# Kernel tuning notes

Hardware: AMD Instinct MI355X
Metric: run time of the kernel (lower is better)

The kernel has to match this reference:

```python
import jax, jax.numpy as jnp
import numpy as np

N = 8192      # nodes
E = 262144    # edges (avg degree 32)
IN_DIM = 512
H1 = 256
H2 = 128


def _graph_conv(x, src, dst, W, b, act):
    """DGL GraphConv with norm='both', allow_zero_in_degree=True.
    h = D_in^{-1/2} * A @ (D_out^{-1/2} * x @ W) + b, then activation.
    Degrees clamped to min 1 (DGL behavior)."""
    ones = jnp.ones((src.shape[0],), dtype=x.dtype)
    deg_out = jax.ops.segment_sum(ones, src, num_segments=N)
    deg_in = jax.ops.segment_sum(ones, dst, num_segments=N)
    norm_src = jnp.maximum(deg_out, 1.0) ** -0.5  # [N]
    norm_dst = jnp.maximum(deg_in, 1.0) ** -0.5   # [N]
    # apply weight before aggregation (out_feats < in_feats, as DGL does)
    h = (x * norm_src[:, None]) @ W               # [N, out]
    agg = jax.ops.segment_sum(h[src], dst, num_segments=N)  # gather-scatter SpMM
    return act(agg * norm_dst[:, None] + b)


def setup_inputs() -> dict:
    key = jax.random.key(0)
    ks = jax.random.split(key, 7)
    features = jax.random.normal(ks[0], (N, IN_DIM), dtype=jnp.float32)
    src = jax.random.randint(ks[1], (E,), 0, N)
    dst = jax.random.randint(ks[2], (E,), 0, N)
    W1 = jax.random.normal(ks[3], (IN_DIM, H1), dtype=jnp.float32) * (1.0 / np.sqrt(IN_DIM))
    b1 = jnp.zeros((H1,), dtype=jnp.float32)
    W2 = jax.random.normal(ks[4], (H1, H2), dtype=jnp.float32) * (1.0 / np.sqrt(H1))
    b2 = jnp.zeros((H2,), dtype=jnp.float32)
    return {"features": features, "src": src, "dst": dst,
            "W1": W1, "b1": b1, "W2": W2, "b2": b2}


def reference(features, src, dst, W1, b1, W2, b2):
    x = _graph_conv(features, src, dst, W1, b1, jax.nn.relu)
    emb = _graph_conv(x, src, dst, W2, b2, lambda a: a)
    logits = jax.nn.sigmoid(emb @ emb.T)  # [N, N] dense reconstruction
    return (emb, logits)
```

## Files before the change

### kernel.cpp

```cpp
#include <hip/hip_runtime.h>

#define NN 8192
#define EE 262144
#define IN_DIM 512
#define HD1 256
#define HD2 128

typedef __attribute__((ext_vector_type(8))) short bf16x8;
typedef __attribute__((ext_vector_type(4))) float f32x4;

__device__ inline unsigned short f2bf(float f) {
    unsigned int u = __builtin_bit_cast(unsigned int, f);
    u += 0x7fffu + ((u >> 16) & 1u);
    return (unsigned short)(u >> 16);
}


__global__ void deg_kernel(const int* __restrict__ src, const int* __restrict__ dst,
                           int* __restrict__ deg_out, int* __restrict__ deg_in) {
    int e = blockIdx.x * blockDim.x + threadIdx.x;
    if (e < EE) {
        atomicAdd(&deg_out[src[e]], 1);
        atomicAdd(&deg_in[dst[e]], 1);
    }
}

__global__ void norm_kernel(const int* __restrict__ deg_out, const int* __restrict__ deg_in,
                            float* __restrict__ norm_src, float* __restrict__ norm_dst) {
    int i = blockIdx.x * blockDim.x + threadIdx.x;
    if (i < NN) {
        int dout = deg_out[i]; if (dout < 1) dout = 1;
        int din  = deg_in[i];  if (din  < 1) din  = 1;
        norm_src[i] = rsqrtf((float)dout);
        norm_dst[i] = rsqrtf((float)din);
    }
}

__global__ void scan_kernel(const int* __restrict__ counts, int* __restrict__ row_start) {
    __shared__ int sums[256];
    int t = threadIdx.x;
    int base = t * 32;
    int local[32];
    int s = 0;
    for (int i = 0; i < 32; i++) { local[i] = s; s += counts[base + i]; }
    sums[t] = s;
    __syncthreads();
    for (int off = 1; off < 256; off <<= 1) {
        int v = (t >= off) ? sums[t - off] : 0;
        __syncthreads();
        sums[t] += v;
        __syncthreads();
    }
    int coff = (t == 0) ? 0 : sums[t - 1];
    for (int i = 0; i < 32; i++) row_start[base + i] = coff + local[i];
    if (t == 255) row_start[NN] = sums[255];
}

__global__ void fill_kernel(const int* __restrict__ src, const int* __restrict__ dst,
                            const int* __restrict__ row_start, int* __restrict__ cursor,
                            int* __restrict__ eidx) {
    int e = blockIdx.x * blockDim.x + threadIdx.x;
    if (e < EE) {
        int d = dst[e];
        int pos = atomicAdd(&cursor[d], 1);
        eidx[row_start[d] + pos] = src[e];
    }
}


__global__ void scale_cast_kernel(const float4* __restrict__ x, const float* __restrict__ norm_src,
                                  ushort4* __restrict__ out) {
    int idx = blockIdx.x * blockDim.x + threadIdx.x;
    if (idx < NN * IN_DIM / 4) {
        float ns = norm_src[idx >> 7];
        float4 v = x[idx];
        ushort4 o;
        o.x = f2bf(v.x * ns); o.y = f2bf(v.y * ns);
        o.z = f2bf(v.z * ns); o.w = f2bf(v.w * ns);
        out[idx] = o;
    }
}

__global__ void transpose_cast_kernel(const float* __restrict__ W, unsigned short* __restrict__ Wt,
                                      int K, int Nc) {
    int idx = blockIdx.x * blockDim.x + threadIdx.x;
    if (idx < K * Nc) {
        int n = idx / K;
        int k = idx - n * K;
        Wt[idx] = f2bf(W[k * Nc + n]);
    }
}

template <int EPI>
__global__ __launch_bounds__(256) void gemm_tn(const short* __restrict__ A,
                                               const short* __restrict__ B,
                                               float* __restrict__ C, int N, int K) {
    int wave = threadIdx.x >> 6;
    int lane = threadIdx.x & 63;
    int wr = wave >> 1, wc = wave & 1;
    int row0 = blockIdx.y * 128 + wr * 64;
    int col0 = blockIdx.x * 128 + wc * 64;
    int l15 = lane & 15, q = lane >> 4;

    f32x4 acc[4][4] = {};
    const short* Abase = A + (size_t)(row0 + l15) * K + q * 8;
    const short* Bbase = B + (size_t)(col0 + l15) * K + q * 8;
    int nk = K >> 5;
    for (int ks = 0; ks < nk; ks++) {
        bf16x8 a[4], b[4];
#pragma unroll
        for (int t = 0; t < 4; t++) {
            a[t] = *(const bf16x8*)(Abase + (size_t)t * 16 * K + ks * 32);
            b[t] = *(const bf16x8*)(Bbase + (size_t)t * 16 * K + ks * 32);
        }
#pragma unroll
        for (int ti = 0; ti < 4; ti++)
#pragma unroll
            for (int tj = 0; tj < 4; tj++)
                acc[ti][tj] = __builtin_amdgcn_mfma_f32_16x16x32_bf16(a[ti], b[tj], acc[ti][tj], 0, 0, 0);
    }
#pragma unroll
    for (int ti = 0; ti < 4; ti++) {
#pragma unroll
        for (int tj = 0; tj < 4; tj++) {
#pragma unroll
            for (int r = 0; r < 4; r++) {
                int row = row0 + ti * 16 + q * 4 + r;
                int col = col0 + tj * 16 + l15;
                float v = acc[ti][tj][r];
                if (EPI == 1) v = __builtin_amdgcn_rcpf(1.0f + __expf(-v));
                C[(size_t)row * N + col] = v;
            }
        }
    }
}


__global__ void spmm1_kernel(const float* __restrict__ h1, const int* __restrict__ row_start,
                             const int* __restrict__ eidx, const float* __restrict__ norm_dst,
                             const float* __restrict__ norm_src, const float* __restrict__ b1,
                             unsigned short* __restrict__ x1n) {
    int r = blockIdx.x;
    int t = threadIdx.x;
    int s = row_start[r], e = row_start[r + 1];
    float sum = 0.0f;
    int i = s;
    for (; i + 4 <= e; i += 4) {
        int n0 = eidx[i], n1 = eidx[i + 1], n2 = eidx[i + 2], n3 = eidx[i + 3];
        float v0 = h1[n0 * HD1 + t];
        float v1 = h1[n1 * HD1 + t];
        float v2 = h1[n2 * HD1 + t];
        float v3 = h1[n3 * HD1 + t];
        sum += v0 + v1 + v2 + v3;
    }
    for (; i < e; i++) sum += h1[eidx[i] * HD1 + t];
    float x = sum * norm_dst[r] + b1[t];
    x = fmaxf(x, 0.0f) * norm_src[r];
    x1n[r * HD1 + t] = f2bf(x);
}

__global__ void spmm2_kernel(const float* __restrict__ h2, const int* __restrict__ row_start,
                             const int* __restrict__ eidx, const float* __restrict__ norm_dst,
                             const float* __restrict__ b2, float* __restrict__ emb,
                             unsigned short* __restrict__ embb) {
    int r = blockIdx.x;
    int t = threadIdx.x;
    int s = row_start[r], e = row_start[r + 1];
    float sum = 0.0f;
    int i = s;
    for (; i + 4 <= e; i += 4) {
        int n0 = eidx[i], n1 = eidx[i + 1], n2 = eidx[i + 2], n3 = eidx[i + 3];
        float v0 = h2[n0 * HD2 + t];
        float v1 = h2[n1 * HD2 + t];
        float v2 = h2[n2 * HD2 + t];
        float v3 = h2[n3 * HD2 + t];
        sum += v0 + v1 + v2 + v3;
    }
    for (; i < e; i++) sum += h2[eidx[i] * HD2 + t];
    float x = sum * norm_dst[r] + b2[t];
    emb[r * HD2 + t] = x;
    embb[r * HD2 + t] = f2bf(x);
}


extern "C" void kernel_launch(void* const* d_in, const int* in_sizes, int n_in,
                              void* d_out, int out_size, void* d_ws, size_t ws_size,
                              hipStream_t stream) {
    const float* features = (const float*)d_in[0];
    const int* src = (const int*)d_in[1];
    const int* dst = (const int*)d_in[2];
    const float* W1 = (const float*)d_in[3];
    const float* b1 = (const float*)d_in[4];
    const float* W2 = (const float*)d_in[5];
    const float* b2 = (const float*)d_in[6];

    char* ws = (char*)d_ws;
    size_t o = 0;
    auto alloc = [&](size_t bytes) -> char* {
        char* p = ws + o;
        o = (o + bytes + 255) & ~(size_t)255;
        return p;
    };
    int* deg_out = (int*)alloc(NN * 4);
    int* deg_in  = (int*)alloc(NN * 4);
    int* cursor  = (int*)alloc(NN * 4);
    float* norm_src = (float*)alloc(NN * 4);
    float* norm_dst = (float*)alloc(NN * 4);
    int* row_start  = (int*)alloc((NN + 1) * 4);
    int* eidx       = (int*)alloc(EE * 4);
    unsigned short* xn  = (unsigned short*)alloc((size_t)NN * IN_DIM * 2);
    unsigned short* w1t = (unsigned short*)alloc((size_t)HD1 * IN_DIM * 2);
    unsigned short* w2t = (unsigned short*)alloc((size_t)HD2 * HD1 * 2);
    float* h1 = (float*)alloc((size_t)NN * HD1 * 4);
    unsigned short* x1n = (unsigned short*)alloc((size_t)NN * HD1 * 2);
    float* h2 = (float*)alloc((size_t)NN * HD2 * 4);
    unsigned short* embb = (unsigned short*)alloc((size_t)NN * HD2 * 2);

    float* emb_out = (float*)d_out;
    float* logits_out = emb_out + (size_t)NN * HD2;

    hipMemsetAsync(deg_out, 0, (size_t)NN * 4 * 3, stream);

    deg_kernel<<<EE / 256, 256, 0, stream>>>(src, dst, deg_out, deg_in);
    norm_kernel<<<NN / 256, 256, 0, stream>>>(deg_out, deg_in, norm_src, norm_dst);
    scan_kernel<<<1, 256, 0, stream>>>(deg_in, row_start);
    fill_kernel<<<EE / 256, 256, 0, stream>>>(src, dst, row_start, cursor, eidx);

    scale_cast_kernel<<<(NN * IN_DIM / 4) / 256, 256, 0, stream>>>(
        (const float4*)features, norm_src, (ushort4*)xn);
    transpose_cast_kernel<<<(IN_DIM * HD1 + 255) / 256, 256, 0, stream>>>(W1, w1t, IN_DIM, HD1);
    transpose_cast_kernel<<<(HD1 * HD2 + 255) / 256, 256, 0, stream>>>(W2, w2t, HD1, HD2);

    gemm_tn<0><<<dim3(HD1 / 128, NN / 128), 256, 0, stream>>>(
        (const short*)xn, (const short*)w1t, h1, HD1, IN_DIM);
    spmm1_kernel<<<NN, HD1, 0, stream>>>(h1, row_start, eidx, norm_dst, norm_src, b1, x1n);

    gemm_tn<0><<<dim3(HD2 / 128, NN / 128), 256, 0, stream>>>(
        (const short*)x1n, (const short*)w2t, h2, HD2, HD1);
    spmm2_kernel<<<NN, HD2, 0, stream>>>(h2, row_start, eidx, norm_dst, b2, emb_out, embb);

    gemm_tn<1><<<dim3(NN / 128, NN / 128), 256, 0, stream>>>(
        (const short*)embb, (const short*)embb, logits_out, NN, HD2);
}
```

Measured before the change: 434.8 us.

## Stage GEMM epilogue through LDS for coalesced stores; vectorize SpMM with wave-per-row

The GEMM epilogue now writes accumulators to shared memory in two halves and then emits coalesced 16-byte row stores, using nontemporal stores for the large sigmoid logits output. The SpMM kernels switch from one block per row with scalar gathers to one wave per row, with float4/float2 vector gathers and vector stores. The aim is to cut write transactions on the 256MB logits output and raise gather efficiency. The cost is extra LDS traffic and barriers in the epilogue.

```diff
diff --git a/kernel.cpp b/kernel.cpp
--- a/kernel.cpp
+++ b/kernel.cpp
@@ -95,6 +95,7 @@
 __global__ __launch_bounds__(256) void gemm_tn(const short* __restrict__ A,
                                                const short* __restrict__ B,
                                                float* __restrict__ C, int N, int K) {
+    __shared__ float lds[64][132];
     int wave = threadIdx.x >> 6;
     int lane = threadIdx.x & 63;
     int wr = wave >> 1, wc = wave & 1;
@@ -119,67 +120,112 @@
             for (int tj = 0; tj < 4; tj++)
                 acc[ti][tj] = __builtin_amdgcn_mfma_f32_16x16x32_bf16(a[ti], b[tj], acc[ti][tj], 0, 0, 0);
     }
-#pragma unroll
-    for (int ti = 0; ti < 4; ti++) {
-#pragma unroll
-        for (int tj = 0; tj < 4; tj++) {
-#pragma unroll
-            for (int r = 0; r < 4; r++) {
-                int row = row0 + ti * 16 + q * 4 + r;
-                int col = col0 + tj * 16 + l15;
-                float v = acc[ti][tj][r];
-                if (EPI == 1) v = __builtin_amdgcn_rcpf(1.0f + __expf(-v));
-                C[(size_t)row * N + col] = v;
+
+    int brow = blockIdx.y * 128;
+    int bcol = blockIdx.x * 128;
+#pragma unroll
+    for (int h = 0; h < 2; h++) {
+        __syncthreads();
+        if (wr == h) {
+#pragma unroll
+            for (int ti = 0; ti < 4; ti++)
+#pragma unroll
+                for (int tj = 0; tj < 4; tj++)
+#pragma unroll
+                    for (int r = 0; r < 4; r++)
+                        lds[ti * 16 + q * 4 + r][wc * 64 + tj * 16 + l15] = acc[ti][tj][r];
+        }
+        __syncthreads();
+#pragma unroll
+        for (int it = 0; it < 8; it++) {
+            int idx = it * 256 + threadIdx.x;
+            int rl = idx >> 5;
+            int c4 = (idx & 31) << 2;
+            f32x4 v = *(const f32x4*)&lds[rl][c4];
+            float* dst = C + (size_t)(brow + h * 64 + rl) * N + bcol + c4;
+            if (EPI == 1) {
+                f32x4 s;
+                s[0] = __builtin_amdgcn_rcpf(1.0f + __expf(-v[0]));
+                s[1] = __builtin_amdgcn_rcpf(1.0f + __expf(-v[1]));
+                s[2] = __builtin_amdgcn_rcpf(1.0f + __expf(-v[2]));
+                s[3] = __builtin_amdgcn_rcpf(1.0f + __expf(-v[3]));
+                __builtin_nontemporal_store(s, (f32x4*)dst);
+            } else {
+                *(f32x4*)dst = v;
             }
         }
     }
 }
 
 
-__global__ void spmm1_kernel(const float* __restrict__ h1, const int* __restrict__ row_start,
-                             const int* __restrict__ eidx, const float* __restrict__ norm_dst,
-                             const float* __restrict__ norm_src, const float* __restrict__ b1,
-                             unsigned short* __restrict__ x1n) {
-    int r = blockIdx.x;
-    int t = threadIdx.x;
+__global__ __launch_bounds__(256) void spmm1_kernel(
+        const float* __restrict__ h1, const int* __restrict__ row_start,
+        const int* __restrict__ eidx, const float* __restrict__ norm_dst,
+        const float* __restrict__ norm_src, const float* __restrict__ b1,
+        unsigned short* __restrict__ x1n) {
+    int wave = threadIdx.x >> 6, lane = threadIdx.x & 63;
+    int r = blockIdx.x * 4 + wave;
     int s = row_start[r], e = row_start[r + 1];
-    float sum = 0.0f;
+    const float* hb = h1 + (size_t)lane * 4;
+    float sx = 0.f, sy = 0.f, sz = 0.f, sw = 0.f;
     int i = s;
     for (; i + 4 <= e; i += 4) {
         int n0 = eidx[i], n1 = eidx[i + 1], n2 = eidx[i + 2], n3 = eidx[i + 3];
-        float v0 = h1[n0 * HD1 + t];
-        float v1 = h1[n1 * HD1 + t];
-        float v2 = h1[n2 * HD1 + t];
-        float v3 = h1[n3 * HD1 + t];
-        sum += v0 + v1 + v2 + v3;
-    }
-    for (; i < e; i++) sum += h1[eidx[i] * HD1 + t];
-    float x = sum * norm_dst[r] + b1[t];
-    x = fmaxf(x, 0.0f) * norm_src[r];
-    x1n[r * HD1 + t] = f2bf(x);
-}
-
-__global__ void spmm2_kernel(const float* __restrict__ h2, const int* __restrict__ row_start,
-                             const int* __restrict__ eidx, const float* __restrict__ norm_dst,
-                             const float* __restrict__ b2, float* __restrict__ emb,
-                             unsigned short* __restrict__ embb) {
-    int r = blockIdx.x;
-    int t = threadIdx.x;
+        float4 v0 = *(const float4*)(hb + (size_t)n0 * HD1);
+        float4 v1 = *(const float4*)(hb + (size_t)n1 * HD1);
+        float4 v2 = *(const float4*)(hb + (size_t)n2 * HD1);
+        float4 v3 = *(const float4*)(hb + (size_t)n3 * HD1);
+        sx += (v0.x + v1.x) + (v2.x + v3.x);
+        sy += (v0.y + v1.y) + (v2.y + v3.y);
+        sz += (v0.z + v1.z) + (v2.z + v3.z);
+        sw += (v0.w + v1.w) + (v2.w + v3.w);
+    }
+    for (; i < e; i++) {
+        float4 v = *(const float4*)(hb + (size_t)eidx[i] * HD1);
+        sx += v.x; sy += v.y; sz += v.z; sw += v.w;
+    }
+    float nd = norm_dst[r], ns = norm_src[r];
+    float4 bb = *(const float4*)(b1 + lane * 4);
+    ushort4 o;
+    o.x = f2bf(fmaxf(sx * nd + bb.x, 0.f) * ns);
+    o.y = f2bf(fmaxf(sy * nd + bb.y, 0.f) * ns);
+    o.z = f2bf(fmaxf(sz * nd + bb.z, 0.f) * ns);
+    o.w = f2bf(fmaxf(sw * nd + bb.w, 0.f) * ns);
+    *(ushort4*)(x1n + (size_t)r * HD1 + lane * 4) = o;
+}
+
+__global__ __launch_bounds__(256) void spmm2_kernel(
+        const float* __restrict__ h2, const int* __restrict__ row_start,
+        const int* __restrict__ eidx, const float* __restrict__ norm_dst,
+        const float* __restrict__ b2, float* __restrict__ emb,
+        unsigned short* __restrict__ embb) {
+    int wave = threadIdx.x >> 6, lane = threadIdx.x & 63;
+    int r = blockIdx.x * 4 + wave;
     int s = row_start[r], e = row_start[r + 1];
-    float sum = 0.0f;
+    const float* hb = h2 + (size_t)lane * 2;
+    float sx = 0.f, sy = 0.f;
     int i = s;
     for (; i + 4 <= e; i += 4) {
         int n0 = eidx[i], n1 = eidx[i + 1], n2 = eidx[i + 2], n3 = eidx[i + 3];
-        float v0 = h2[n0 * HD2 + t];
-        float v1 = h2[n1 * HD2 + t];
-        float v2 = h2[n2 * HD2 + t];
-        float v3 = h2[n3 * HD2 + t];
-        sum += v0 + v1 + v2 + v3;
-    }
-    for (; i < e; i++) sum += h2[eidx[i] * HD2 + t];
-    float x = sum * norm_dst[r] + b2[t];
-    emb[r * HD2 + t] = x;
-    embb[r * HD2 + t] = f2bf(x);
+        float2 v0 = *(const float2*)(hb + (size_t)n0 * HD2);
+        float2 v1 = *(const float2*)(hb + (size_t)n1 * HD2);
+        float2 v2 = *(const float2*)(hb + (size_t)n2 * HD2);
+        float2 v3 = *(const float2*)(hb + (size_t)n3 * HD2);
+        sx += (v0.x + v1.x) + (v2.x + v3.x);
+        sy += (v0.y + v1.y) + (v2.y + v3.y);
+    }
+    for (; i < e; i++) {
+        float2 v = *(const float2*)(hb + (size_t)eidx[i] * HD2);
+        sx += v.x; sy += v.y;
+    }
+    float nd = norm_dst[r];
+    float2 bb = *(const float2*)(b2 + lane * 2);
+    float x0 = sx * nd + bb.x;
+    float x1 = sy * nd + bb.y;
+    float2 ov; ov.x = x0; ov.y = x1;
+    *(float2*)(emb + (size_t)r * HD2 + lane * 2) = ov;
+    ushort2 ob; ob.x = f2bf(x0); ob.y = f2bf(x1);
+    *(ushort2*)(embb + (size_t)r * HD2 + lane * 2) = ob;
 }
 
 
@@ -219,7 +265,7 @@
     float* emb_out = (float*)d_out;
     float* logits_out = emb_out + (size_t)NN * HD2;
 
-    hipMemsetAsync(deg_out, 0, (size_t)NN * 4 * 3, stream);
+    (void)hipMemsetAsync(deg_out, 0, (size_t)NN * 4 * 3, stream);
 
     deg_kernel<<<EE / 256, 256, 0, stream>>>(src, dst, deg_out, deg_in);
     norm_kernel<<<NN / 256, 256, 0, stream>>>(deg_out, deg_in, norm_src, norm_dst);
@@ -233,11 +279,11 @@
 
     gemm_tn<0><<<dim3(HD1 / 128, NN / 128), 256, 0, stream>>>(
         (const short*)xn, (const short*)w1t, h1, HD1, IN_DIM);
-    spmm1_kernel<<<NN, HD1, 0, stream>>>(h1, row_start, eidx, norm_dst, norm_src, b1, x1n);
+    spmm1_kernel<<<NN / 4, 256, 0, stream>>>(h1, row_start, eidx, norm_dst, norm_src, b1, x1n);
 
     gemm_tn<0><<<dim3(HD2 / 128, NN / 128), 256, 0, stream>>>(
         (const short*)x1n, (const short*)w2t, h2, HD2, HD1);
-    spmm2_kernel<<<NN, HD2, 0, stream>>>(h2, row_start, eidx, norm_dst, b2, emb_out, embb);
+    spmm2_kernel<<<NN / 4, 256, 0, stream>>>(h2, row_start, eidx, norm_dst, b2, emb_out, embb);
 
     gemm_tn<1><<<dim3(NN / 128, NN / 128), 256, 0, stream>>>(
         (const short*)embb, (const short*)embb, logits_out, NN, HD2);
```

New measurement: 428.5 us. Within noise of the previous version (-1.5%).
